# Kernel tuning notes

Hardware: AMD Instinct MI355X
Metric: run time of the kernel (lower is better)

Reference implementation:

```python
import jax, jax.numpy as jnp
import numpy as np


def setup_inputs() -> dict:
    key = jax.random.key(0)
    x = jax.random.normal(key, (4, 256, 64, 64), dtype=jnp.float32)
    return {"x": x}


def reference(x):
    # x: [B, C, W, H]
    B, C, W, H = x.shape
    N = W * H
    q = x.reshape(B, C, N).transpose(0, 2, 1)  # [B, N, C] (proj_query)
    # per-token L2 norm over channels
    q_norm = jnp.linalg.norm(q, ord=2, axis=2)  # [B, N]
    # outer product of norms: [B, N, N]
    nm = q_norm[:, :, None] * q_norm[:, None, :]
    # raw dot-product energy: [B, N, N]
    energy = jnp.einsum('bnc,bmc->bnm', q, q)
    norm_energy = energy / (nm + 1e-6)
    attention = jax.nn.softmax(norm_energy, axis=-1)
    return attention
```

## Files before the change

kernel.cpp:

```cpp
#include <hip/hip_runtime.h>
#include <hip/hip_bf16.h>

#define BATCH 4
#define CDIM  256
#define NTOK  4096

#define BM 64
#define BN 256

typedef short bf16x8 __attribute__((ext_vector_type(8)));
typedef float floatx4 __attribute__((ext_vector_type(4)));
typedef unsigned int uintx4 __attribute__((ext_vector_type(4)));
typedef unsigned int u32;

#define PIN(v) asm volatile("" : "+v"(v))
#define WAIT(n) asm volatile("s_waitcnt vmcnt(" #n ")" ::: "memory")
#define BAR() do { __builtin_amdgcn_s_barrier(); asm volatile("" ::: "memory"); } while (0)

__device__ inline u32 f2bf1(float f) {
    u32 u = __float_as_uint(f);
    u += 0x7fffu + ((u >> 16) & 1u);
    return u >> 16;
}
__device__ inline u32 f2bf2(float lo, float hi) { return f2bf1(lo) | (f2bf1(hi) << 16); }

__device__ inline void gload_lds16(const short* g, short* l) {
    __builtin_amdgcn_global_load_lds(
        (const __attribute__((address_space(1))) u32*)g,
        (__attribute__((address_space(3))) u32*)l, 16, 0, 0);
}

#define TT 32
__global__ __launch_bounds__(256) void prep_kernel(const float* __restrict__ x,
                                                   short* __restrict__ xn) {
    __shared__ float tile[TT][CDIM + 2];
    __shared__ float part[8][TT];
    __shared__ float rinv_s[TT];
    const int tid = threadIdx.x;
    const int blk = blockIdx.x;
    const int b = blk >> 7;
    const int t0 = (blk & 127) * TT;
    const float* xb = x + (size_t)b * CDIM * NTOK;
    const int ti = tid & 31, cq = tid >> 5;
    float ss = 0.f;
    for (int c = cq; c < CDIM; c += 8) {
        float v = xb[(size_t)c * NTOK + t0 + ti];
        tile[ti][c] = v;
        ss += v * v;
    }
    part[cq][ti] = ss;
    __syncthreads();
    if (tid < TT) {
        float s = 0.f;
#pragma unroll
        for (int q = 0; q < 8; ++q) s += part[q][tid];
        rinv_s[tid] = 1.0f / sqrtf(s);
    }
    __syncthreads();
    const int tok = tid >> 3, seg = tid & 7;
    const float ri = rinv_s[tok];
    size_t obase = ((size_t)(b * NTOK + t0 + tok)) * CDIM + seg * 32;
#pragma unroll
    for (int j = 0; j < 4; ++j) {
        u32 w[4];
#pragma unroll
        for (int u = 0; u < 4; ++u) {
            float f0 = tile[tok][seg * 32 + j * 8 + 2 * u] * ri;
            float f1 = tile[tok][seg * 32 + j * 8 + 2 * u + 1] * ri;
            w[u] = f2bf2(f0, f1);
        }
        *(uintx4*)&xn[obase + j * 8] = (uintx4){w[0], w[1], w[2], w[3]};
    }
}

__global__ __launch_bounds__(512, 2) void attn_kernel(const short* __restrict__ xn,
                                                      float* __restrict__ out) {
    __shared__ short Bs[4][256][64];
    __shared__ float rowsumLds[BM][8];
    const int tid = threadIdx.x;
    const int D = blockIdx.x;
    const int b = D >> 6;
    const int rb = (D & 63) * BM;
    const short* xnb = xn + (size_t)b * NTOK * CDIM;
    float* outb = out + ((size_t)b << 24);
    const int lane = tid & 63, wid = tid >> 6;
    const int wcol = wid << 5;
    const int r0 = lane & 15, kq = lane >> 4;
    const int sx = r0 & 7;
    const int tr0 = wcol + r0, tr1 = wcol + 16 + r0;

    const int trl = (wid << 3) + (lane >> 3);
    const int c8 = (lane & 7) ^ (lane >> 3);

    bf16x8 afr[4][8];
#pragma unroll
    for (int m = 0; m < 4; ++m) {
        const short* arow = xnb + (size_t)(rb + m * 16 + r0) * CDIM;
#pragma unroll
        for (int j = 0; j < 8; ++j) {
            afr[m][j] = *(const bf16x8*)(arow + j * 32 + kq * 8);
            PIN(afr[m][j]);
        }
    }

    float psum[16];
#pragma unroll
    for (int i = 0; i < 16; ++i) psum[i] = 0.f;
    floatx4 acc[4][2];

    auto stage = [&](int ct, int kc) {
        const short* s0 = xnb + (size_t)(ct * BN + trl) * CDIM + kc * 64 + c8 * 8;
        short* d = &Bs[kc][wid << 3][0];
#pragma unroll
        for (int rr = 0; rr < 4; ++rr)
            gload_lds16(s0 + (size_t)(rr * 64) * CDIM, d + rr * 64 * 64);
    };

#define ACCZERO() do { _Pragma("unroll") for (int m = 0; m < 4; ++m) { \
        acc[m][0] = (floatx4){0,0,0,0}; acc[m][1] = (floatx4){0,0,0,0}; } } while (0)

#define COMPUTE(KC) do { \
    __builtin_amdgcn_s_setprio(1); \
    const int p0 = kq ^ sx, p1 = (4 | kq) ^ sx; \
    bf16x8 b00 = *(const bf16x8*)&Bs[KC][tr0][p0 * 8]; \
    bf16x8 b10 = *(const bf16x8*)&Bs[KC][tr1][p0 * 8]; \
    bf16x8 b01 = *(const bf16x8*)&Bs[KC][tr0][p1 * 8]; \
    bf16x8 b11 = *(const bf16x8*)&Bs[KC][tr1][p1 * 8]; \
    _Pragma("unroll") for (int m = 0; m < 4; ++m) \
        acc[m][0] = __builtin_amdgcn_mfma_f32_16x16x32_bf16(afr[m][(KC)*2], b00, acc[m][0], 0,0,0); \
    _Pragma("unroll") for (int m = 0; m < 4; ++m) \
        acc[m][1] = __builtin_amdgcn_mfma_f32_16x16x32_bf16(afr[m][(KC)*2], b10, acc[m][1], 0,0,0); \
    _Pragma("unroll") for (int m = 0; m < 4; ++m) \
        acc[m][0] = __builtin_amdgcn_mfma_f32_16x16x32_bf16(afr[m][(KC)*2+1], b01, acc[m][0], 0,0,0); \
    _Pragma("unroll") for (int m = 0; m < 4; ++m) \
        acc[m][1] = __builtin_amdgcn_mfma_f32_16x16x32_bf16(afr[m][(KC)*2+1], b11, acc[m][1], 0,0,0); \
    __builtin_amdgcn_s_setprio(0); \
} while (0)

#define STEP(KC, SCT, SKC, WN) do { stage((SCT), (SKC)); WAIT(WN); BAR(); COMPUTE(KC); } while (0)
#define STEPNS(KC, WN)        do { WAIT(WN); BAR(); COMPUTE(KC); } while (0)

#define EPI0() do { \
    _Pragma("unroll") for (int m = 0; m < 4; ++m) \
    _Pragma("unroll") for (int r = 0; r < 4; ++r) \
        psum[m * 4 + r] += __expf(acc[m][0][r] - 1.f) + __expf(acc[m][1][r] - 1.f); \
} while (0)

#define EPI1(CT) do { \
    _Pragma("unroll") for (int m = 0; m < 4; ++m) \
    _Pragma("unroll") for (int r = 0; r < 4; ++r) { \
        const int row = rb + m * 16 + kq * 4 + r; \
        float* p = outb + ((size_t)row << 12) + ((CT) << 8) + wcol + r0; \
        const float ri = psum[m * 4 + r]; \
        __builtin_nontemporal_store(__expf(acc[m][0][r] - 1.f) * ri, p); \
        __builtin_nontemporal_store(__expf(acc[m][1][r] - 1.f) * ri, p + 16); } \
} while (0)

    stage(0, 0); stage(0, 1);
    for (int ct = 0; ct < 15; ++ct) {
        ACCZERO();
        STEP(0, ct, 2, 8);
        STEP(1, ct, 3, 8);
        STEP(2, ct + 1, 0, 8);
        STEP(3, ct + 1, 1, 8);
        EPI0();
    }
    ACCZERO();
    STEP(0, 15, 2, 8);
    STEP(1, 15, 3, 8);
    STEPNS(2, 4);
    STEPNS(3, 0);
    EPI0();

#pragma unroll
    for (int m = 0; m < 4; ++m)
#pragma unroll
        for (int r = 0; r < 4; ++r) {
            float v = psum[m * 4 + r];
            v += __shfl_xor(v, 1); v += __shfl_xor(v, 2);
            v += __shfl_xor(v, 4); v += __shfl_xor(v, 8);
            if (r0 == 0) rowsumLds[m * 16 + kq * 4 + r][wid] = v;
        }
    __syncthreads();
#pragma unroll
    for (int m = 0; m < 4; ++m)
#pragma unroll
        for (int r = 0; r < 4; ++r) {
            const int row = m * 16 + kq * 4 + r;
            float s = 0.f;
#pragma unroll
            for (int w = 0; w < 8; ++w) s += rowsumLds[row][w];
            psum[m * 4 + r] = 1.0f / s;
        }
    __syncthreads();

    stage(0, 0); stage(0, 1);
    {
        ACCZERO();
        STEP(0, 0, 2, 8);
        STEP(1, 0, 3, 8);
        STEP(2, 1, 0, 8);
        STEP(3, 1, 1, 8);
        EPI1(0);
    }
    for (int ct = 1; ct < 15; ++ct) {
        ACCZERO();
        STEP(0, ct, 2, 40);
        STEP(1, ct, 3, 40);
        STEP(2, ct + 1, 0, 8);
        STEP(3, ct + 1, 1, 8);
        EPI1(ct);
    }
    ACCZERO();
    STEP(0, 15, 2, 40);
    STEP(1, 15, 3, 40);
    STEPNS(2, 4);
    STEPNS(3, 0);
    EPI1(15);

#undef ACCZERO
#undef COMPUTE
#undef STEP
#undef STEPNS
#undef EPI0
#undef EPI1
}

extern "C" void kernel_launch(void* const* d_in, const int* in_sizes, int n_in,
                              void* d_out, int out_size, void* d_ws, size_t ws_size,
                              hipStream_t stream) {
    const float* x = (const float*)d_in[0];
    float* out = (float*)d_out;
    short* xn = (short*)d_ws;

    prep_kernel<<<BATCH * (NTOK / TT), 256, 0, stream>>>(x, xn);
    attn_kernel<<<NTOK / BM * BATCH, 512, 0, stream>>>(xn, out);
}
```

Before: 154.3 us.

## Software-pipeline LDS fragment reads ahead of MFMA with deeper staging

Restructures the K-chunk loop so the B fragments for the next chunk are read from LDS into registers before the barrier, while the MFMAs for the current chunk run after a single lgkmcnt wait. Global-to-LDS staging now runs three chunks ahead instead of two, and wait counts are retuned to match. The goal is to hide LDS read latency and cut barrier stalls. In exchange it uses more registers, and with a 4-slot buffer ring the ordering between overwriting a slot and finishing reads from it becomes tight.

New measurement: 159.9 us. 1.04x slower.

```diff
diff --git a/kernel.cpp b/kernel.cpp
--- a/kernel.cpp
+++ b/kernel.cpp
@@ -15,6 +15,7 @@
 
 #define PIN(v) asm volatile("" : "+v"(v))
 #define WAIT(n) asm volatile("s_waitcnt vmcnt(" #n ")" ::: "memory")
+#define LGKM0() asm volatile("s_waitcnt lgkmcnt(0)" ::: "memory")
 #define BAR() do { __builtin_amdgcn_s_barrier(); asm volatile("" ::: "memory"); } while (0)
 
 __device__ inline u32 f2bf1(float f) {
@@ -107,6 +108,7 @@
 #pragma unroll
     for (int i = 0; i < 16; ++i) psum[i] = 0.f;
     floatx4 acc[4][2];
+    bf16x8 nb00, nb10, nb01, nb11;
 
     auto stage = [&](int ct, int kc) {
         const short* s0 = xnb + (size_t)(ct * BN + trl) * CDIM + kc * 64 + c8 * 8;
@@ -119,26 +121,28 @@
 #define ACCZERO() do { _Pragma("unroll") for (int m = 0; m < 4; ++m) { \
         acc[m][0] = (floatx4){0,0,0,0}; acc[m][1] = (floatx4){0,0,0,0}; } } while (0)
 
-#define COMPUTE(KC) do { \
+#define DSREAD(KC) do { \
+    const int p0 = kq ^ sx, p1 = (4 | kq) ^ sx; \
+    nb00 = *(const bf16x8*)&Bs[KC][tr0][p0 * 8]; \
+    nb10 = *(const bf16x8*)&Bs[KC][tr1][p0 * 8]; \
+    nb01 = *(const bf16x8*)&Bs[KC][tr0][p1 * 8]; \
+    nb11 = *(const bf16x8*)&Bs[KC][tr1][p1 * 8]; \
+} while (0)
+
+#define MFMA16(KC) do { \
+    LGKM0(); \
+    __builtin_amdgcn_sched_barrier(0); \
     __builtin_amdgcn_s_setprio(1); \
-    const int p0 = kq ^ sx, p1 = (4 | kq) ^ sx; \
-    bf16x8 b00 = *(const bf16x8*)&Bs[KC][tr0][p0 * 8]; \
-    bf16x8 b10 = *(const bf16x8*)&Bs[KC][tr1][p0 * 8]; \
-    bf16x8 b01 = *(const bf16x8*)&Bs[KC][tr0][p1 * 8]; \
-    bf16x8 b11 = *(const bf16x8*)&Bs[KC][tr1][p1 * 8]; \
-    _Pragma("unroll") for (int m = 0; m < 4; ++m) \
-        acc[m][0] = __builtin_amdgcn_mfma_f32_16x16x32_bf16(afr[m][(KC)*2], b00, acc[m][0], 0,0,0); \
-    _Pragma("unroll") for (int m = 0; m < 4; ++m) \
-        acc[m][1] = __builtin_amdgcn_mfma_f32_16x16x32_bf16(afr[m][(KC)*2], b10, acc[m][1], 0,0,0); \
-    _Pragma("unroll") for (int m = 0; m < 4; ++m) \
-        acc[m][0] = __builtin_amdgcn_mfma_f32_16x16x32_bf16(afr[m][(KC)*2+1], b01, acc[m][0], 0,0,0); \
-    _Pragma("unroll") for (int m = 0; m < 4; ++m) \
-        acc[m][1] = __builtin_amdgcn_mfma_f32_16x16x32_bf16(afr[m][(KC)*2+1], b11, acc[m][1], 0,0,0); \
+    _Pragma("unroll") for (int m = 0; m < 4; ++m) \
+        acc[m][0] = __builtin_amdgcn_mfma_f32_16x16x32_bf16(afr[m][(KC)*2], nb00, acc[m][0], 0,0,0); \
+    _Pragma("unroll") for (int m = 0; m < 4; ++m) \
+        acc[m][1] = __builtin_amdgcn_mfma_f32_16x16x32_bf16(afr[m][(KC)*2], nb10, acc[m][1], 0,0,0); \
+    _Pragma("unroll") for (int m = 0; m < 4; ++m) \
+        acc[m][0] = __builtin_amdgcn_mfma_f32_16x16x32_bf16(afr[m][(KC)*2+1], nb01, acc[m][0], 0,0,0); \
+    _Pragma("unroll") for (int m = 0; m < 4; ++m) \
+        acc[m][1] = __builtin_amdgcn_mfma_f32_16x16x32_bf16(afr[m][(KC)*2+1], nb11, acc[m][1], 0,0,0); \
     __builtin_amdgcn_s_setprio(0); \
 } while (0)
-
-#define STEP(KC, SCT, SKC, WN) do { stage((SCT), (SKC)); WAIT(WN); BAR(); COMPUTE(KC); } while (0)
-#define STEPNS(KC, WN)        do { WAIT(WN); BAR(); COMPUTE(KC); } while (0)
 
 #define EPI0() do { \
     _Pragma("unroll") for (int m = 0; m < 4; ++m) \
@@ -157,20 +161,20 @@
 } while (0)
 
     stage(0, 0); stage(0, 1);
+    WAIT(4); BAR();
+    DSREAD(0); stage(0, 2);
+    WAIT(4); BAR();
+    ACCZERO();
     for (int ct = 0; ct < 15; ++ct) {
-        ACCZERO();
-        STEP(0, ct, 2, 8);
-        STEP(1, ct, 3, 8);
-        STEP(2, ct + 1, 0, 8);
-        STEP(3, ct + 1, 1, 8);
-        EPI0();
-    }
-    ACCZERO();
-    STEP(0, 15, 2, 8);
-    STEP(1, 15, 3, 8);
-    STEPNS(2, 4);
-    STEPNS(3, 0);
-    EPI0();
+        MFMA16(0); stage(ct, 3);     WAIT(4); DSREAD(1); BAR();
+        MFMA16(1); stage(ct + 1, 0); WAIT(4); DSREAD(2); BAR();
+        MFMA16(2); stage(ct + 1, 1); WAIT(4); DSREAD(3); BAR();
+        MFMA16(3); EPI0(); ACCZERO(); stage(ct + 1, 2); WAIT(4); DSREAD(0); BAR();
+    }
+    MFMA16(0); stage(15, 3); WAIT(4); DSREAD(1); BAR();
+    MFMA16(1); WAIT(0); DSREAD(2); BAR();
+    MFMA16(2); DSREAD(3); BAR();
+    MFMA16(3); EPI0();
 
 #pragma unroll
     for (int m = 0; m < 4; ++m)
@@ -195,33 +199,30 @@
     __syncthreads();
 
     stage(0, 0); stage(0, 1);
+    WAIT(4); BAR();
+    DSREAD(0); stage(0, 2);
+    WAIT(4); BAR();
+    ACCZERO();
     {
-        ACCZERO();
-        STEP(0, 0, 2, 8);
-        STEP(1, 0, 3, 8);
-        STEP(2, 1, 0, 8);
-        STEP(3, 1, 1, 8);
-        EPI1(0);
+        MFMA16(0); stage(0, 3); WAIT(4); DSREAD(1); BAR();
+        MFMA16(1); stage(1, 0); WAIT(4); DSREAD(2); BAR();
+        MFMA16(2); stage(1, 1); WAIT(4); DSREAD(3); BAR();
+        MFMA16(3); stage(1, 2); EPI1(0); ACCZERO(); WAIT(36); DSREAD(0); BAR();
     }
     for (int ct = 1; ct < 15; ++ct) {
-        ACCZERO();
-        STEP(0, ct, 2, 40);
-        STEP(1, ct, 3, 40);
-        STEP(2, ct + 1, 0, 8);
-        STEP(3, ct + 1, 1, 8);
-        EPI1(ct);
-    }
-    ACCZERO();
-    STEP(0, 15, 2, 40);
-    STEP(1, 15, 3, 40);
-    STEPNS(2, 4);
-    STEPNS(3, 0);
-    EPI1(15);
+        MFMA16(0); stage(ct, 3);     WAIT(36); DSREAD(1); BAR();
+        MFMA16(1); stage(ct + 1, 0); WAIT(4);  DSREAD(2); BAR();
+        MFMA16(2); stage(ct + 1, 1); WAIT(4);  DSREAD(3); BAR();
+        MFMA16(3); stage(ct + 1, 2); EPI1(ct); ACCZERO(); WAIT(36); DSREAD(0); BAR();
+    }
+    MFMA16(0); stage(15, 3); WAIT(36); DSREAD(1); BAR();
+    MFMA16(1); WAIT(0); DSREAD(2); BAR();
+    MFMA16(2); DSREAD(3); BAR();
+    MFMA16(3); EPI1(15);
 
 #undef ACCZERO
-#undef COMPUTE
-#undef STEP
-#undef STEPNS
+#undef DSREAD
+#undef MFMA16
 #undef EPI0
 #undef EPI1
 }
```
